# Kernel optimization log

Measured on AMD Instinct MI355X. Metric: run time of the kernel, lower is better.

Reference implementation:

```python
import math
import jax, jax.numpy as jnp
import numpy as np

FACTOR = 5


def setup_inputs() -> dict:
    key = jax.random.key(0)
    kq, kk, kv, ki = jax.random.split(key, 4)
    B, H, L, D = 4, 8, 2048, 64
    sample_k = min(FACTOR * math.ceil(math.log(L)), L)  # 40
    queries = jax.random.normal(kq, (B, H, L, D), dtype=jnp.float32)
    keys = jax.random.normal(kk, (B, H, L, D), dtype=jnp.float32)
    values = jax.random.normal(kv, (B, H, L, D), dtype=jnp.float32)
    index_sample = jax.random.randint(ki, (L, sample_k), 0, L, dtype=jnp.int64 if jax.config.jax_enable_x64 else jnp.int32)
    return {"queries": queries, "keys": keys, "values": values, "index_sample": index_sample}


def reference(queries, keys, values, index_sample):
    B, H, L_Q, D = queries.shape
    L_K = keys.shape[2]
    u = min(FACTOR * math.ceil(math.log(L_Q)), L_Q)  # n_top queries (= 40)
    scale = 1.0 / math.sqrt(D)

    # --- _prob_QK: sparsity measurement over randomly sampled keys ---
    # K_sample[b,h,q,s,:] = keys[b,h,index_sample[q,s],:]  -> [B,H,L_Q,S,D]
    K_sample = keys[:, :, index_sample, :]
    Q_K_sample = jnp.einsum('bhqd,bhqsd->bhqs', queries, K_sample)  # [B,H,L_Q,S]
    M = Q_K_sample.max(axis=-1) - Q_K_sample.sum(axis=-1) / L_K      # [B,H,L_Q]
    _, M_top = jax.lax.top_k(M, u)                                    # [B,H,u]

    Q_reduce = jnp.take_along_axis(queries, M_top[..., None], axis=2)  # [B,H,u,D]
    scores_top = jnp.einsum('bhud,bhkd->bhuk', Q_reduce, keys) * scale  # [B,H,u,L_K]

    # --- initial context: causal cumulative sum of V (mask_flag=True) ---
    context = jnp.cumsum(values, axis=2)  # [B,H,L_Q,D]

    # --- ProbMask: causal rows gathered at the selected query indices ---
    causal = jnp.triu(jnp.ones((L_Q, L_K), dtype=bool), 1)  # [L_Q,L_K]
    mask = causal[M_top]                                     # [B,H,u,L_K]
    scores_top = jnp.where(mask, -jnp.inf, scores_top)

    attn = jax.nn.softmax(scores_top, axis=-1)                       # [B,H,u,L_K]
    update = jnp.einsum('bhuk,bhkd->bhud', attn, values)             # [B,H,u,D]

    b_idx = jnp.arange(B)[:, None, None]
    h_idx = jnp.arange(H)[None, :, None]
    context = context.at[b_idx, h_idx, M_top].set(update.astype(context.dtype))
    return context
```

## Files before the change

### kernel.cpp

```cpp
#include <hip/hip_runtime.h>
#include <math.h>

#define BB 4
#define HH 8
#define LL 2048
#define DD 64
#define SK 40
#define BH (BB*HH)
#define NC 8

__device__ __forceinline__ unsigned ordu(float v) {
    unsigned u = __float_as_uint(v);
    return (u & 0x80000000u) ? ~u : (u | 0x80000000u);
}

__global__ __launch_bounds__(256) void stage1_kernel(
        const float* __restrict__ Q, const float* __restrict__ K,
        const float* __restrict__ V, const int* __restrict__ IDX,
        float* __restrict__ M, float* __restrict__ csum) {
    int tid = threadIdx.x;
    if (blockIdx.x < 1024) {
        int x = blockIdx.x;
        int bhLo = x & 7;
        int r = x >> 3;
        int bhHi = r & 3;
        int chunk = r >> 2;
        int bh = bhHi * 8 + bhLo;
        int qbase = chunk * 64;
        int w = tid >> 6, lane = tid & 63;
        int qw = lane >> 2, c = lane & 3;
        int qi = w * 16 + qw;
        int qpos = qbase + qi;

        __shared__ int sidx[64 * SK];
        for (int i = tid; i < 64 * SK; i += 256) sidx[i] = IDX[(size_t)qbase * SK + i];

        const float4* Q4 = (const float4*)Q;
        const float4* K4 = (const float4*)K;
        float4 qreg[4];
        #pragma unroll
        for (int j = 0; j < 4; ++j)
            qreg[j] = Q4[((size_t)bh * LL + qpos) * 16 + j * 4 + c];
        __syncthreads();

        size_t kb4 = (size_t)bh * LL * 16;
        float mx = -INFINITY, sm = 0.f;
        #pragma unroll 8
        for (int s = 0; s < SK; ++s) {
            int ks = sidx[qi * SK + s];
            const float4* kr = K4 + kb4 + (size_t)ks * 16;
            float p = 0.f;
            #pragma unroll
            for (int j = 0; j < 4; ++j) {
                float4 kv = kr[j * 4 + c];
                p += qreg[j].x * kv.x + qreg[j].y * kv.y + qreg[j].z * kv.z + qreg[j].w * kv.w;
            }
            p += __shfl_xor(p, 1, 64);
            p += __shfl_xor(p, 2, 64);
            mx = fmaxf(mx, p);
            sm += p;
        }
        if (c == 0) M[(size_t)bh * LL + qpos] = mx - sm * (1.0f / (float)LL);
    } else {
        int x = blockIdx.x - 1024;
        int bhLo = x & 7, r = x >> 3;
        int bhHi = r & 3, c = r >> 2;
        int bh = bhHi * 8 + bhLo;
        int d = tid & 63, sg = tid >> 6;
        size_t base = (size_t)bh * LL * DD;
        int row0 = c * 128 + sg * 32;
        float s = 0.f;
        for (int j = 0; j < 32; ++j) s += V[base + (size_t)(row0 + j) * DD + d];
        __shared__ float part[4][DD];
        part[sg][d] = s;
        __syncthreads();
        if (sg == 0)
            csum[((size_t)bh * 16 + c) * DD + d] = part[0][d] + part[1][d] + part[2][d] + part[3][d];
    }
}

__global__ __launch_bounds__(256) void stage2_kernel(
        const float* __restrict__ V, const float* __restrict__ csum,
        const float* __restrict__ M, float* __restrict__ out,
        int* __restrict__ topk) {
    int tid = threadIdx.x;
    if (blockIdx.x < 512) {
        int x = blockIdx.x;
        int bhLo = x & 7, r = x >> 3;
        int bhHi = r & 3, c = r >> 2;
        int bh = bhHi * 8 + bhLo;
        int d = tid & 63, sg = tid >> 6;
        size_t base = (size_t)bh * LL * DD;
        int row0 = c * 128 + sg * 32;
        float v[32];
        #pragma unroll
        for (int j = 0; j < 32; ++j) v[j] = V[base + (size_t)(row0 + j) * DD + d];
        float s = 0.f;
        #pragma unroll
        for (int j = 0; j < 32; ++j) s += v[j];
        __shared__ float part[4][DD];
        part[sg][d] = s;
        __syncthreads();
        float pre = 0.f;
        for (int cc = 0; cc < c; ++cc) pre += csum[((size_t)bh * 16 + cc) * DD + d];
        for (int ss = 0; ss < sg; ++ss) pre += part[ss][d];
        float acc = pre;
        #pragma unroll
        for (int j = 0; j < 32; ++j) {
            acc += v[j];
            out[base + (size_t)(row0 + j) * DD + d] = acc;
        }
    } else {
        int bh = blockIdx.x - 512;
        __shared__ unsigned hist[256];
        __shared__ unsigned bc_prefix, bc_need;
        __shared__ unsigned cnt_gt, cnt_eq;
        __shared__ int eqlist[128];

        unsigned v[8];
        #pragma unroll
        for (int j = 0; j < 8; ++j)
            v[j] = ordu(M[(size_t)bh * LL + tid + j * 256]);

        unsigned prefix = 0, need = SK;
        #pragma unroll
        for (int pass = 0; pass < 4; ++pass) {
            const int s = 24 - 8 * pass;
            const unsigned maskHigh = (pass == 0) ? 0u : (0xFFFFFFFFu << (s + 8));
            hist[tid] = 0;
            __syncthreads();
            #pragma unroll
            for (int j = 0; j < 8; ++j)
                if (((v[j] ^ prefix) & maskHigh) == 0)
                    atomicAdd(&hist[(v[j] >> s) & 0xFF], 1u);
            __syncthreads();
            unsigned above = 0;
            for (int b = tid + 1; b < 256; ++b) above += hist[b];
            if (above < need && above + hist[tid] >= need) {
                bc_prefix = prefix | ((unsigned)tid << s);
                bc_need = need - above;
            }
            __syncthreads();
            prefix = bc_prefix;
            need = bc_need;
            __syncthreads();
        }
        unsigned T = prefix;
        if (tid == 0) { cnt_gt = 0; cnt_eq = 0; }
        __syncthreads();
        #pragma unroll
        for (int j = 0; j < 8; ++j) {
            int idx = tid + j * 256;
            if (v[j] > T) { unsigned p = atomicAdd(&cnt_gt, 1u); topk[bh * SK + p] = idx; }
            else if (v[j] == T) { unsigned p = atomicAdd(&cnt_eq, 1u); if (p < 128) eqlist[p] = idx; }
        }
        __syncthreads();
        if (tid == 0) {
            int ne = (int)min(cnt_eq, 128u);
            unsigned base = cnt_gt;
            for (unsigned r2 = 0; r2 < need; ++r2) {
                int bj = 0, bv = 0x7FFFFFFF;
                for (int j = 0; j < ne; ++j)
                    if (eqlist[j] < bv) { bv = eqlist[j]; bj = j; }
                topk[bh * SK + base + r2] = bv;
                eqlist[bj] = 0x7FFFFFFF;
            }
        }
    }
}

__global__ __launch_bounds__(256) void attn_kernel(
        const float* __restrict__ Q, const float* __restrict__ K,
        const float* __restrict__ V, const int* __restrict__ topk,
        float* __restrict__ pm, float* __restrict__ pl,
        float* __restrict__ po) {
    int x = blockIdx.x;
    int bhLo = x & 7;
    int r = x >> 3;
    int c = r & 7;
    r >>= 3;
    int u = r % SK;
    int bhHi = r / SK;
    int bh = bhHi * 8 + bhLo;
    int g = bh * SK + u;
    int tid = threadIdx.x;

    int qpos = topk[g];
    int nk = qpos + 1;
    int cl = (nk + NC - 1) >> 3;
    int k0 = c * cl;
    int len = min(cl, nk - k0);
    if (len <= 0) return;

    __shared__ float sc[256];
    __shared__ float red[4], red2[4];
    __shared__ float opart[16][16][4];

    size_t pbase = (size_t)g * NC + c;

    int w = tid >> 6, lane = tid & 63;
    int kw = lane >> 2, cc = lane & 3;
    const float4* Q4 = (const float4*)Q;
    const float4* K4 = (const float4*)K;
    const float4* V4 = (const float4*)V;
    float4 qreg[4];
    #pragma unroll
    for (int j = 0; j < 4; ++j)
        qreg[j] = Q4[((size_t)bh * LL + qpos) * 16 + j * 4 + cc];

    size_t kb4 = (size_t)bh * LL * 16;
    int rounds = (len + 63) >> 6;
    for (int rr = 0; rr < rounds; ++rr) {
        int j = rr * 64 + w * 16 + kw;
        if (j < len) {
            const float4* kr = K4 + kb4 + (size_t)(k0 + j) * 16;
            float p = 0.f;
            #pragma unroll
            for (int jj = 0; jj < 4; ++jj) {
                float4 kv = kr[jj * 4 + cc];
                p += qreg[jj].x * kv.x + qreg[jj].y * kv.y + qreg[jj].z * kv.z + qreg[jj].w * kv.w;
            }
            p += __shfl_xor(p, 1, 64);
            p += __shfl_xor(p, 2, 64);
            if (cc == 0) sc[j] = p * 0.125f;
        }
    }
    __syncthreads();

    float m = (tid < len) ? sc[tid] : -INFINITY;
    #pragma unroll
    for (int off = 32; off > 0; off >>= 1) m = fmaxf(m, __shfl_xor(m, off, 64));
    if (lane == 0) red[w] = m;
    __syncthreads();
    m = fmaxf(fmaxf(red[0], red[1]), fmaxf(red[2], red[3]));

    float e = 0.f;
    if (tid < len) {
        e = expf(sc[tid] - m);
        sc[tid] = e;
    }
    #pragma unroll
    for (int off = 32; off > 0; off >>= 1) e += __shfl_xor(e, off, 64);
    if (lane == 0) red2[w] = e;
    __syncthreads();
    float lsum = red2[0] + red2[1] + red2[2] + red2[3];

    int col4 = tid & 15, kg = tid >> 4;
    float ax = 0.f, ay = 0.f, az = 0.f, aw = 0.f;
    for (int j = kg; j < len; j += 16) {
        float sj = sc[j];
        float4 vv = V4[((size_t)bh * LL + k0 + j) * 16 + col4];
        ax += sj * vv.x; ay += sj * vv.y; az += sj * vv.z; aw += sj * vv.w;
    }
    opart[kg][col4][0] = ax;
    opart[kg][col4][1] = ay;
    opart[kg][col4][2] = az;
    opart[kg][col4][3] = aw;
    __syncthreads();
    if (tid < DD) {
        int c4 = tid >> 2, cp = tid & 3;
        float s = 0.f;
        #pragma unroll
        for (int kg2 = 0; kg2 < 16; ++kg2) s += opart[kg2][c4][cp];
        po[pbase * DD + tid] = s;
    }
    if (tid == 0) { pm[pbase] = m; pl[pbase] = lsum; }
}

__global__ __launch_bounds__(256) void combine_kernel(
        const float* __restrict__ pm, const float* __restrict__ pl,
        const float* __restrict__ po, const int* __restrict__ topk,
        float* __restrict__ out) {
    int g = blockIdx.x * 4 + (threadIdx.x >> 6);
    int d = threadIdx.x & 63;
    int qpos = topk[g];
    int bh = g / SK;
    int nk = qpos + 1;
    int cl = (nk + NC - 1) >> 3;
    int ncv = (nk + cl - 1) / cl;
    size_t gb = (size_t)g * NC;
    float gm = -INFINITY;
    for (int j = 0; j < ncv; ++j) gm = fmaxf(gm, pm[gb + j]);
    float L = 0.f, o = 0.f;
    for (int j = 0; j < ncv; ++j) {
        float wj = expf(pm[gb + j] - gm);
        L += pl[gb + j] * wj;
        o += po[(gb + j) * DD + d] * wj;
    }
    out[((size_t)bh * LL + qpos) * DD + d] = o / L;
}

extern "C" void kernel_launch(void* const* d_in, const int* in_sizes, int n_in,
                              void* d_out, int out_size, void* d_ws, size_t ws_size,
                              hipStream_t stream) {
    const float* Q   = (const float*)d_in[0];
    const float* K   = (const float*)d_in[1];
    const float* V   = (const float*)d_in[2];
    const int*   IDX = (const int*)d_in[3];
    float* out = (float*)d_out;

    char* ws = (char*)d_ws;
    float* M    = (float*)ws;  ws += (size_t)BH * LL * sizeof(float);
    int*   topk = (int*)ws;    ws += ((size_t)BH * SK * sizeof(int) + 255) & ~255ull;
    float* csum = (float*)ws;  ws += (size_t)BH * 16 * DD * sizeof(float);
    float* pm   = (float*)ws;  ws += ((size_t)BH * SK * NC * sizeof(float) + 255) & ~255ull;
    float* pl   = (float*)ws;  ws += ((size_t)BH * SK * NC * sizeof(float) + 255) & ~255ull;
    float* po   = (float*)ws;

    stage1_kernel<<<1536, 256, 0, stream>>>(Q, K, V, IDX, M, csum);
    stage2_kernel<<<544, 256, 0, stream>>>(V, csum, M, out, topk);
    attn_kernel<<<BH * SK * NC, 256, 0, stream>>>(Q, K, V, topk, pm, pl, po);
    combine_kernel<<<BH * SK / 4, 256, 0, stream>>>(pm, pl, po, topk, out);
}
```

Before: 168.1 us.

## Batch all top queries per key chunk in attention kernel to reuse K/V loads

The attention kernel no longer launches one block per (query, chunk). Each block now takes a fixed 128-key chunk of one head and computes scores for all 40 selected queries. Q rows are staged in shared memory, and each K and V row is read once per chunk and reused across the 40 queries, so far fewer blocks launch and redundant K/V global traffic drops. The combine step now handles fully masked chunks, and stage1 batches four gathered K-row loads per step to raise memory-level parallelism. The trade-off is that blocks whose chunk is causally masked for many queries do wasted or idle work, and the new kernel uses more shared memory and registers.

```diff
diff --git a/kernel.cpp b/kernel.cpp
--- a/kernel.cpp
+++ b/kernel.cpp
@@ -7,7 +7,8 @@
 #define DD 64
 #define SK 40
 #define BH (BB*HH)
-#define NC 8
+#define NC 16
+#define CK 128
 
 __device__ __forceinline__ unsigned ordu(float v) {
     unsigned u = __float_as_uint(v);
@@ -45,20 +46,28 @@
 
         size_t kb4 = (size_t)bh * LL * 16;
         float mx = -INFINITY, sm = 0.f;
-        #pragma unroll 8
-        for (int s = 0; s < SK; ++s) {
-            int ks = sidx[qi * SK + s];
-            const float4* kr = K4 + kb4 + (size_t)ks * 16;
-            float p = 0.f;
-            #pragma unroll
-            for (int j = 0; j < 4; ++j) {
-                float4 kv = kr[j * 4 + c];
-                p += qreg[j].x * kv.x + qreg[j].y * kv.y + qreg[j].z * kv.z + qreg[j].w * kv.w;
-            }
-            p += __shfl_xor(p, 1, 64);
-            p += __shfl_xor(p, 2, 64);
-            mx = fmaxf(mx, p);
-            sm += p;
+        #pragma unroll
+        for (int s0 = 0; s0 < SK; s0 += 4) {
+            float4 kv[4][4];
+            #pragma unroll
+            for (int t = 0; t < 4; ++t) {
+                int ks = sidx[qi * SK + s0 + t];
+                const float4* kr = K4 + kb4 + (size_t)ks * 16;
+                #pragma unroll
+                for (int j = 0; j < 4; ++j) kv[t][j] = kr[j * 4 + c];
+            }
+            #pragma unroll
+            for (int t = 0; t < 4; ++t) {
+                float p = 0.f;
+                #pragma unroll
+                for (int j = 0; j < 4; ++j)
+                    p += qreg[j].x * kv[t][j].x + qreg[j].y * kv[t][j].y
+                       + qreg[j].z * kv[t][j].z + qreg[j].w * kv[t][j].w;
+                p += __shfl_xor(p, 1, 64);
+                p += __shfl_xor(p, 2, 64);
+                mx = fmaxf(mx, p);
+                sm += p;
+            }
         }
         if (c == 0) M[(size_t)bh * LL + qpos] = mx - sm * (1.0f / (float)LL);
     } else {
@@ -177,94 +186,118 @@
     int x = blockIdx.x;
     int bhLo = x & 7;
     int r = x >> 3;
-    int c = r & 7;
-    r >>= 3;
-    int u = r % SK;
-    int bhHi = r / SK;
+    int c = r & 15;
+    int bhHi = r >> 4;
     int bh = bhHi * 8 + bhLo;
-    int g = bh * SK + u;
     int tid = threadIdx.x;
-
-    int qpos = topk[g];
-    int nk = qpos + 1;
-    int cl = (nk + NC - 1) >> 3;
-    int k0 = c * cl;
-    int len = min(cl, nk - k0);
-    if (len <= 0) return;
-
-    __shared__ float sc[256];
-    __shared__ float red[4], red2[4];
-    __shared__ float opart[16][16][4];
-
-    size_t pbase = (size_t)g * NC + c;
-
     int w = tid >> 6, lane = tid & 63;
-    int kw = lane >> 2, cc = lane & 3;
+    int cbase = c * CK;
+
+    __shared__ int qp[SK];
+    __shared__ float4 sq4[SK][16];
+    __shared__ float SC[CK][SK + 1];
+
+    if (tid < SK) qp[tid] = topk[bh * SK + tid];
+    __syncthreads();
     const float4* Q4 = (const float4*)Q;
     const float4* K4 = (const float4*)K;
     const float4* V4 = (const float4*)V;
-    float4 qreg[4];
-    #pragma unroll
-    for (int j = 0; j < 4; ++j)
-        qreg[j] = Q4[((size_t)bh * LL + qpos) * 16 + j * 4 + cc];
-
-    size_t kb4 = (size_t)bh * LL * 16;
-    int rounds = (len + 63) >> 6;
-    for (int rr = 0; rr < rounds; ++rr) {
-        int j = rr * 64 + w * 16 + kw;
-        if (j < len) {
-            const float4* kr = K4 + kb4 + (size_t)(k0 + j) * 16;
-            float p = 0.f;
-            #pragma unroll
-            for (int jj = 0; jj < 4; ++jj) {
-                float4 kv = kr[jj * 4 + cc];
-                p += qreg[jj].x * kv.x + qreg[jj].y * kv.y + qreg[jj].z * kv.z + qreg[jj].w * kv.w;
-            }
+    for (int i = tid; i < SK * 16; i += 256) {
+        int u = i >> 4, j = i & 15;
+        sq4[u][j] = Q4[((size_t)bh * LL + qp[u]) * 16 + j];
+    }
+    __syncthreads();
+
+    {
+        int half = tid & 1;
+        int kk = tid >> 1;
+        int kg = cbase + kk;
+        size_t kb4 = (size_t)bh * LL * 16;
+        float4 kreg[8];
+        const float4* kr = K4 + kb4 + (size_t)kg * 16 + half * 8;
+        #pragma unroll
+        for (int j = 0; j < 8; ++j) kreg[j] = kr[j];
+        #pragma unroll 4
+        for (int u = 0; u < SK; ++u) {
+            int qpu = qp[u];
+            if (cbase > qpu) {
+                if (half == 0) SC[kk][u] = -INFINITY;
+                continue;
+            }
+            float pa = 0.f, pb = 0.f;
+            #pragma unroll
+            for (int j = 0; j < 4; ++j) {
+                float4 qv = sq4[u][half * 8 + j];
+                pa += kreg[j].x * qv.x + kreg[j].y * qv.y + kreg[j].z * qv.z + kreg[j].w * qv.w;
+            }
+            #pragma unroll
+            for (int j = 4; j < 8; ++j) {
+                float4 qv = sq4[u][half * 8 + j];
+                pb += kreg[j].x * qv.x + kreg[j].y * qv.y + kreg[j].z * qv.z + kreg[j].w * qv.w;
+            }
+            float p = pa + pb;
             p += __shfl_xor(p, 1, 64);
-            p += __shfl_xor(p, 2, 64);
-            if (cc == 0) sc[j] = p * 0.125f;
+            if (half == 0) SC[kk][u] = (kg <= qpu) ? p * 0.125f : -INFINITY;
         }
     }
     __syncthreads();
 
-    float m = (tid < len) ? sc[tid] : -INFINITY;
-    #pragma unroll
-    for (int off = 32; off > 0; off >>= 1) m = fmaxf(m, __shfl_xor(m, off, 64));
-    if (lane == 0) red[w] = m;
+    for (int u = w; u < SK; u += 4) {
+        float s0 = SC[lane][u], s1 = SC[lane + 64][u];
+        float m = fmaxf(s0, s1);
+        #pragma unroll
+        for (int off = 32; off > 0; off >>= 1) m = fmaxf(m, __shfl_xor(m, off, 64));
+        float e0 = 0.f, e1 = 0.f;
+        if (m != -INFINITY) {
+            e0 = expf(s0 - m);
+            e1 = expf(s1 - m);
+        }
+        SC[lane][u] = e0;
+        SC[lane + 64][u] = e1;
+        float ls = e0 + e1;
+        #pragma unroll
+        for (int off = 32; off > 0; off >>= 1) ls += __shfl_xor(ls, off, 64);
+        if (lane == 0) {
+            size_t pb = (size_t)(bh * SK + u) * NC + c;
+            pm[pb] = m;
+            pl[pb] = ls;
+        }
+    }
     __syncthreads();
-    m = fmaxf(fmaxf(red[0], red[1]), fmaxf(red[2], red[3]));
-
-    float e = 0.f;
-    if (tid < len) {
-        e = expf(sc[tid] - m);
-        sc[tid] = e;
-    }
-    #pragma unroll
-    for (int off = 32; off > 0; off >>= 1) e += __shfl_xor(e, off, 64);
-    if (lane == 0) red2[w] = e;
-    __syncthreads();
-    float lsum = red2[0] + red2[1] + red2[2] + red2[3];
-
-    int col4 = tid & 15, kg = tid >> 4;
-    float ax = 0.f, ay = 0.f, az = 0.f, aw = 0.f;
-    for (int j = kg; j < len; j += 16) {
-        float sj = sc[j];
-        float4 vv = V4[((size_t)bh * LL + k0 + j) * 16 + col4];
-        ax += sj * vv.x; ay += sj * vv.y; az += sj * vv.z; aw += sj * vv.w;
-    }
-    opart[kg][col4][0] = ax;
-    opart[kg][col4][1] = ay;
-    opart[kg][col4][2] = az;
-    opart[kg][col4][3] = aw;
-    __syncthreads();
-    if (tid < DD) {
-        int c4 = tid >> 2, cp = tid & 3;
-        float s = 0.f;
-        #pragma unroll
-        for (int kg2 = 0; kg2 < 16; ++kg2) s += opart[kg2][c4][cp];
-        po[pbase * DD + tid] = s;
-    }
-    if (tid == 0) { pm[pbase] = m; pl[pbase] = lsum; }
+
+    {
+        int ks = tid & 3;
+        int dg = (tid >> 2) & 15;
+        int ug = tid >> 6;
+        int u0 = ug * 10;
+        float4 acc[10];
+        #pragma unroll
+        for (int i = 0; i < 10; ++i) acc[i] = make_float4(0.f, 0.f, 0.f, 0.f);
+        for (int t = 0; t < CK / 4; ++t) {
+            int k = t * 4 + ks;
+            float4 vv = V4[((size_t)bh * LL + cbase + k) * 16 + dg];
+            #pragma unroll
+            for (int i = 0; i < 10; ++i) {
+                float pw = SC[k][u0 + i];
+                acc[i].x += pw * vv.x; acc[i].y += pw * vv.y;
+                acc[i].z += pw * vv.z; acc[i].w += pw * vv.w;
+            }
+        }
+        #pragma unroll
+        for (int i = 0; i < 10; ++i) {
+            acc[i].x += __shfl_xor(acc[i].x, 1, 64); acc[i].x += __shfl_xor(acc[i].x, 2, 64);
+            acc[i].y += __shfl_xor(acc[i].y, 1, 64); acc[i].y += __shfl_xor(acc[i].y, 2, 64);
+            acc[i].z += __shfl_xor(acc[i].z, 1, 64); acc[i].z += __shfl_xor(acc[i].z, 2, 64);
+            acc[i].w += __shfl_xor(acc[i].w, 1, 64); acc[i].w += __shfl_xor(acc[i].w, 2, 64);
+        }
+        if (ks == 0) {
+            #pragma unroll
+            for (int i = 0; i < 10; ++i) {
+                float4* dst = (float4*)&po[((size_t)(bh * SK + u0 + i) * NC + c) * DD + dg * 4];
+                *dst = acc[i];
+            }
+        }
+    }
 }
 
 __global__ __launch_bounds__(256) void combine_kernel(
@@ -275,15 +308,15 @@
     int d = threadIdx.x & 63;
     int qpos = topk[g];
     int bh = g / SK;
-    int nk = qpos + 1;
-    int cl = (nk + NC - 1) >> 3;
-    int ncv = (nk + cl - 1) / cl;
     size_t gb = (size_t)g * NC;
     float gm = -INFINITY;
-    for (int j = 0; j < ncv; ++j) gm = fmaxf(gm, pm[gb + j]);
+    #pragma unroll
+    for (int j = 0; j < NC; ++j) gm = fmaxf(gm, pm[gb + j]);
     float L = 0.f, o = 0.f;
-    for (int j = 0; j < ncv; ++j) {
-        float wj = expf(pm[gb + j] - gm);
+    #pragma unroll
+    for (int j = 0; j < NC; ++j) {
+        float pmj = pm[gb + j];
+        float wj = (pmj == -INFINITY) ? 0.f : expf(pmj - gm);
         L += pl[gb + j] * wj;
         o += po[(gb + j) * DD + d] * wj;
     }
@@ -309,6 +342,6 @@
 
     stage1_kernel<<<1536, 256, 0, stream>>>(Q, K, V, IDX, M, csum);
     stage2_kernel<<<544, 256, 0, stream>>>(V, csum, M, out, topk);
-    attn_kernel<<<BH * SK * NC, 256, 0, stream>>>(Q, K, V, topk, pm, pl, po);
+    attn_kernel<<<BH * NC, 256, 0, stream>>>(Q, K, V, topk, pm, pl, po);
     combine_kernel<<<BH * SK / 4, 256, 0, stream>>>(pm, pl, po, topk, out);
 }
```

Result: faster. 162.7 us (-3.2%).
